# Performance work log

Measured on AMD Instinct MI355X. Metric: run time of the kernel, lower is better.

The kernel has to match this reference:

```python
import jax, jax.numpy as jnp
import numpy as np

B, S, D = 1, 2048, 2048
H, G, HD = 32, 8, 64        # n_heads, n_kv_groups, head_dim
GS = H // G                  # group_size
ROPE_BASE = 10000.0


def _rope_tables(seq_len, head_dim):
    inv_freq = 1.0 / (ROPE_BASE ** (jnp.arange(0, head_dim, 2, dtype=jnp.float32) / head_dim))
    angles = jnp.arange(seq_len, dtype=jnp.float32)[:, None] * inv_freq[None, :]  # [S, HD/2]
    angles = jnp.concatenate([angles, angles], axis=-1)                            # [S, HD]
    return jnp.cos(angles), jnp.sin(angles)


def setup_inputs() -> dict:
    key = jax.random.key(0)
    ks = jax.random.split(key, 5)
    x = jax.random.normal(ks[0], (B, S, D), dtype=jnp.float32)
    mask = jnp.triu(jnp.ones((S, S), dtype=bool), k=1)  # True = masked (causal)
    cos_vals, sin_vals = _rope_tables(S, HD)
    scale = 0.02
    Wq = jax.random.normal(ks[1], (H * HD, D), dtype=jnp.float32) * scale
    Wk = jax.random.normal(ks[2], (G * HD, D), dtype=jnp.float32) * scale
    Wv = jax.random.normal(ks[3], (G * HD, D), dtype=jnp.float32) * scale
    Wo = jax.random.normal(ks[4], (D, H * HD), dtype=jnp.float32) * scale
    return {"x": x, "mask": mask, "cos_vals": cos_vals, "sin_vals": sin_vals,
            "Wq": Wq, "Wk": Wk, "Wv": Wv, "Wo": Wo}


def _apply_rope(t, cos, sin):
    # t: [b, heads, S, HD]; cos/sin: [S, HD]
    half = t.shape[-1] // 2
    t1, t2 = t[..., :half], t[..., half:]
    rotated = jnp.concatenate([-t2, t1], axis=-1)
    return t * cos[None, None] + rotated * sin[None, None]


def reference(x, mask, cos_vals, sin_vals, Wq, Wk, Wv, Wo):
    b, s, _ = x.shape
    q = (x @ Wq.T).reshape(b, s, H, HD).transpose(0, 2, 1, 3)   # [b,H,S,HD]
    k = (x @ Wk.T).reshape(b, s, G, HD).transpose(0, 2, 1, 3)   # [b,G,S,HD]
    v = (x @ Wv.T).reshape(b, s, G, HD).transpose(0, 2, 1, 3)   # [b,G,S,HD]
    q = _apply_rope(q, cos_vals, sin_vals)
    k = _apply_rope(k, cos_vals, sin_vals)
    # Group-broadcast instead of repeat_interleave (same math)
    q = q.reshape(b, G, GS, s, HD)
    scores = jnp.einsum('bghqd,bgkd->bghqk', q, k)              # [b,G,GS,S,S]
    scores = jnp.where(mask[None, None, None], -jnp.inf, scores)
    weights = jax.nn.softmax(scores / np.sqrt(HD).astype(np.float32), axis=-1)
    out = jnp.einsum('bghqk,bgkd->bghqd', weights, v)           # [b,G,GS,S,HD]
    out = out.reshape(b, H, s, HD).transpose(0, 2, 1, 3).reshape(b, s, H * HD)
    return out @ Wo.T
```

## Files before the change

### kernel.cpp

```cpp
#include <hip/hip_runtime.h>
#include <cstddef>
#include <cstdint>

#define S 2048
#define Dm 2048
#define NH 32
#define NG 8
#define HD 64

typedef __attribute__((ext_vector_type(8))) short bf16x8;
typedef __attribute__((ext_vector_type(4))) short bf16x4;
typedef __attribute__((ext_vector_type(4))) float f32x4;

__device__ __forceinline__ float fast_exp2(float x) { return __builtin_amdgcn_exp2f(x); }

__device__ __forceinline__ unsigned short f2bf(float f) {
  unsigned int u = __builtin_bit_cast(unsigned int, f);
  u = (u + 0x7fffu + ((u >> 16) & 1u)) >> 16;
  return (unsigned short)u;
}
__device__ __forceinline__ unsigned int pk2bf(float lo, float hi) {
  unsigned int a = __builtin_bit_cast(unsigned int, lo) + 0x8000u;
  unsigned int b = __builtin_bit_cast(unsigned int, hi) + 0x8000u;
  return (a >> 16) | (b & 0xffff0000u);
}
__device__ __forceinline__ void gl_lds16(const unsigned short* g, unsigned short* l) {
  __builtin_amdgcn_global_load_lds(
      (const __attribute__((address_space(1))) unsigned int*)g,
      (__attribute__((address_space(3))) unsigned int*)l, 16, 0, 0);
}

#define QSC 0.1803368801111601f

__global__ __launch_bounds__(256) void cvt_all(const float* __restrict__ x,
                                               const float* __restrict__ Wq,
                                               const float* __restrict__ Wk,
                                               const float* __restrict__ Wv,
                                               const float* __restrict__ Wo,
                                               unsigned short* __restrict__ xb,
                                               unsigned short* __restrict__ Wcat,
                                               unsigned short* __restrict__ Wob) {
  int i = blockIdx.x * 256 + threadIdx.x;
  const float4* src;
  ushort4* dst;
  if (i < 1048576)      { src = (const float4*)x  + i;             dst = (ushort4*)xb + i; }
  else if (i < 2097152) { src = (const float4*)Wq + (i - 1048576); dst = (ushort4*)Wcat + (i - 1048576); }
  else if (i < 2359296) { src = (const float4*)Wk + (i - 2097152); dst = (ushort4*)Wcat + 1048576 + (i - 2097152); }
  else if (i < 2621440) { src = (const float4*)Wv + (i - 2359296); dst = (ushort4*)Wcat + 1310720 + (i - 2359296); }
  else                  { src = (const float4*)Wo + (i - 2621440); dst = (ushort4*)Wob + (i - 2621440); }
  float4 v = *src;
  ushort4 o;
  o.x = f2bf(v.x); o.y = f2bf(v.y); o.z = f2bf(v.z); o.w = f2bf(v.w);
  *dst = o;
}

__global__ __launch_bounds__(256) void gemm_bf16(const unsigned short* __restrict__ A,
                                                 const unsigned short* __restrict__ B,
                                                 float* __restrict__ Cf,
                                                 unsigned short* __restrict__ Cb,
                                                 unsigned short* __restrict__ VtOut,
                                                 const float* __restrict__ cosv,
                                                 const float* __restrict__ sinv,
                                                 int M, int N, int K) {
  __shared__ __align__(16) unsigned short As[64 * 64];
  __shared__ __align__(16) unsigned short Bs[128 * 64];
  const int tid = threadIdx.x;
  const int lane = tid & 63, wave = tid >> 6;
  const int row0 = blockIdx.y * 64, col0 = blockIdx.x * 128;
  const int wr = (wave >> 1) * 32, wc = (wave & 1) * 64;

  f32x4 acc[2][4];
#pragma unroll
  for (int i = 0; i < 2; i++)
#pragma unroll
    for (int j = 0; j < 4; j++) acc[i][j] = (f32x4){0.f, 0.f, 0.f, 0.f};

  const int arow0 = tid >> 3, aslot0 = ((tid & 7) ^ (arow0 & 7)) * 8;
  const int arow1 = (tid + 256) >> 3, aslot1 = (((tid + 256) & 7) ^ (arow1 & 7)) * 8;
  const int fr = lane & 15, q4 = lane >> 4;

  for (int k0 = 0; k0 < K; k0 += 64) {
    gl_lds16(&A[(size_t)(row0 + arow0) * K + k0 + aslot0], &As[tid * 8]);
    gl_lds16(&A[(size_t)(row0 + arow1) * K + k0 + aslot1], &As[(tid + 256) * 8]);
#pragma unroll
    for (int b = 0; b < 4; b++) {
      int p = tid + b * 256;
      int r = p >> 3, sl = ((p & 7) ^ (r & 7)) * 8;
      gl_lds16(&B[(size_t)(col0 + r) * K + k0 + sl], &Bs[p * 8]);
    }
    __syncthreads();
#pragma unroll
    for (int kk = 0; kk < 2; kk++) {
      bf16x8 af[2], bfr[4];
#pragma unroll
      for (int i = 0; i < 2; i++) {
        int R = wr + i * 16 + fr;
        af[i] = *(const bf16x8*)&As[R * 64 + ((q4 + kk * 4) ^ (R & 7)) * 8];
      }
#pragma unroll
      for (int j = 0; j < 4; j++) {
        int R = wc + j * 16 + fr;
        bfr[j] = *(const bf16x8*)&Bs[R * 64 + ((q4 + kk * 4) ^ (R & 7)) * 8];
      }
#pragma unroll
      for (int i = 0; i < 2; i++)
#pragma unroll
        for (int j = 0; j < 4; j++)
          acc[i][j] = __builtin_amdgcn_mfma_f32_16x16x32_bf16(af[i], bfr[j], acc[i][j], 0, 0, 0);
    }
    __syncthreads();
  }

  const int cc = lane & 15, cr = (lane >> 4) * 4;

  if (cosv) {
#pragma unroll
    for (int i = 0; i < 2; i++) {
      int grb = row0 + wr + i * 16 + cr;
#pragma unroll
      for (int j = 0; j < 2; j++) {
        int gc = col0 + wc + j * 16 + cc;
        if (gc < 2560) {
          int d = j * 16 + cc;
          float qs = (gc < 2048) ? QSC : 1.0f;
#pragma unroll
          for (int r = 0; r < 4; r++) {
            float c = cosv[(grb + r) * 64 + d];
            float s = sinv[(grb + r) * 64 + d];
            float t1 = acc[i][j][r], t2 = acc[i][j + 2][r];
            acc[i][j][r]     = (t1 * c - t2 * s) * qs;
            acc[i][j + 2][r] = (t2 * c + t1 * s) * qs;
          }
        }
      }
    }
  }

#pragma unroll
  for (int i = 0; i < 2; i++)
#pragma unroll
    for (int j = 0; j < 4; j++) {
      int gc = col0 + wc + j * 16 + cc;
#pragma unroll
      for (int r = 0; r < 4; r++) {
        int gr = row0 + wr + i * 16 + cr + r;
        if (cosv) {
          if (gc >= 2560) VtOut[(size_t)(gc - 2560) * 2048 + gr] = f2bf(acc[i][j][r]);
          else            Cb[(size_t)gr * N + gc] = f2bf(acc[i][j][r]);
        } else if (Cf)    Cf[(size_t)gr * N + gc] = acc[i][j][r];
        else              Cb[(size_t)gr * N + gc] = f2bf(acc[i][j][r]);
      }
    }
}

__global__ __launch_bounds__(256, 2) void flash_mfma(const unsigned short* __restrict__ QKV,
                                                     const unsigned short* __restrict__ Vt_g,
                                                     unsigned short* __restrict__ Ob) {
  __shared__ __align__(16) unsigned short Ks[64 * 64];
  __shared__ __align__(16) unsigned short Vs[64 * 64];

  const int tid = threadIdx.x;
  const int lane = tid & 63, wave = tid >> 6;
  const int m15 = lane & 15, q4 = lane >> 4;

  const int L = blockIdx.x;
  const int h = L & 31, g = h >> 2;
  const int u0 = L >> 5, a = u0 >> 3, b = u0 & 7;
  const int u = (a == 0) ? 15 - b : b;
  const int qb = u * 128;
  const int ntiles = 2 * u + 2;

  bf16x8 qf[2][2];
#pragma unroll
  for (int f = 0; f < 2; f++) {
    const size_t qrow = (size_t)(qb + f * 64 + wave * 16 + m15) * 3072 + h * 64;
    qf[f][0] = *(const bf16x8*)&QKV[qrow + q4 * 8];
    qf[f][1] = *(const bf16x8*)&QKV[qrow + 32 + q4 * 8];
  }

  f32x4 accO[2][4];
  float l_i[2] = {0.f, 0.f};
#pragma unroll
  for (int f = 0; f < 2; f++)
#pragma unroll
    for (int v = 0; v < 4; v++) accO[f][v] = (f32x4){0.f, 0.f, 0.f, 0.f};

  const int p0 = wave * 128 + lane, p1 = p0 + 64;
  const int sr0 = p0 >> 3, so0 = ((p0 & 7) ^ (sr0 & 7)) * 8;
  const int sr1 = p1 >> 3, so1 = ((p1 & 7) ^ (sr1 & 7)) * 8;

  for (int t = 0; t < ntiles; t++) {
    const int k0 = t * 64;
    gl_lds16(&QKV[(size_t)(k0 + sr0) * 3072 + 2048 + g * 64 + so0], &Ks[p0 * 8]);
    gl_lds16(&QKV[(size_t)(k0 + sr1) * 3072 + 2048 + g * 64 + so1], &Ks[p1 * 8]);
    gl_lds16(&Vt_g[(size_t)(g * 64 + sr0) * 2048 + k0 + so0], &Vs[p0 * 8]);
    gl_lds16(&Vt_g[(size_t)(g * 64 + sr1) * 2048 + k0 + so1], &Vs[p1 * 8]);
    __syncthreads();

    const bool act0 = (t < ntiles - 1);

    f32x4 sc[2][4];
#pragma unroll
    for (int kt = 0; kt < 4; kt++) {
      const int krow = kt * 16 + m15;
      bf16x8 kf0 = *(const bf16x8*)&Ks[krow * 64 + (q4 ^ (krow & 7)) * 8];
      bf16x8 kf1 = *(const bf16x8*)&Ks[krow * 64 + ((q4 + 4) ^ (krow & 7)) * 8];
      f32x4 z1 = (f32x4){0.f, 0.f, 0.f, 0.f};
      z1 = __builtin_amdgcn_mfma_f32_16x16x32_bf16(kf0, qf[1][0], z1, 0, 0, 0);
      sc[1][kt] = __builtin_amdgcn_mfma_f32_16x16x32_bf16(kf1, qf[1][1], z1, 0, 0, 0);
      if (act0) {
        f32x4 z0 = (f32x4){0.f, 0.f, 0.f, 0.f};
        z0 = __builtin_amdgcn_mfma_f32_16x16x32_bf16(kf0, qf[0][0], z0, 0, 0, 0);
        sc[0][kt] = __builtin_amdgcn_mfma_f32_16x16x32_bf16(kf1, qf[0][1], z0, 0, 0, 0);
      }
    }

    bf16x8 pA0[2], pA1[2];
#pragma unroll
    for (int f = 0; f < 2; f++) {
      if (f == 0 && !act0) continue;
      if (t == 2 * u + f) {
        const int qo = wave * 16 + m15;
#pragma unroll
        for (int kt = 0; kt < 4; kt++)
#pragma unroll
          for (int r = 0; r < 4; r++)
            if (kt * 16 + q4 * 4 + r > qo) sc[f][kt][r] = -1e30f;
      }
      float rs = 0.f;
#pragma unroll
      for (int kt = 0; kt < 4; kt++)
#pragma unroll
        for (int r = 0; r < 4; r++) {
          float p = fast_exp2(sc[f][kt][r]);
          sc[f][kt][r] = p;
          rs += p;
        }
      rs += __shfl_xor(rs, 16);
      rs += __shfl_xor(rs, 32);
      l_i[f] += rs;

      int4 pa0, pa1;
      pa0.x = pk2bf(sc[f][0][0], sc[f][0][1]); pa0.y = pk2bf(sc[f][0][2], sc[f][0][3]);
      pa0.z = pk2bf(sc[f][1][0], sc[f][1][1]); pa0.w = pk2bf(sc[f][1][2], sc[f][1][3]);
      pa1.x = pk2bf(sc[f][2][0], sc[f][2][1]); pa1.y = pk2bf(sc[f][2][2], sc[f][2][3]);
      pa1.z = pk2bf(sc[f][3][0], sc[f][3][1]); pa1.w = pk2bf(sc[f][3][2], sc[f][3][3]);
      pA0[f] = __builtin_bit_cast(bf16x8, pa0);
      pA1[f] = __builtin_bit_cast(bf16x8, pa1);
    }

#pragma unroll
    for (int vt = 0; vt < 4; vt++) {
      const int vrow = vt * 16 + m15;
      const int base = vrow * 64, sw = vrow & 7, half = (q4 & 1) * 4, c1 = q4 >> 1;
      bf16x4 w00 = *(const bf16x4*)&Vs[base + (c1 ^ sw) * 8 + half];
      bf16x4 w01 = *(const bf16x4*)&Vs[base + ((c1 + 2) ^ sw) * 8 + half];
      bf16x4 w10 = *(const bf16x4*)&Vs[base + ((c1 + 4) ^ sw) * 8 + half];
      bf16x4 w11 = *(const bf16x4*)&Vs[base + ((c1 + 6) ^ sw) * 8 + half];
      bf16x8 vB0 = __builtin_shufflevector(w00, w01, 0, 1, 2, 3, 4, 5, 6, 7);
      bf16x8 vB1 = __builtin_shufflevector(w10, w11, 0, 1, 2, 3, 4, 5, 6, 7);
      accO[1][vt] = __builtin_amdgcn_mfma_f32_16x16x32_bf16(pA0[1], vB0, accO[1][vt], 0, 0, 0);
      accO[1][vt] = __builtin_amdgcn_mfma_f32_16x16x32_bf16(pA1[1], vB1, accO[1][vt], 0, 0, 0);
      if (act0) {
        accO[0][vt] = __builtin_amdgcn_mfma_f32_16x16x32_bf16(pA0[0], vB0, accO[0][vt], 0, 0, 0);
        accO[0][vt] = __builtin_amdgcn_mfma_f32_16x16x32_bf16(pA1[0], vB1, accO[0][vt], 0, 0, 0);
      }
    }
    __syncthreads();
  }

#pragma unroll
  for (int f = 0; f < 2; f++) {
    float lr[4];
#pragma unroll
    for (int r = 0; r < 4; r++) lr[r] = 1.0f / __shfl(l_i[f], q4 * 20 + r);
#pragma unroll
    for (int vt = 0; vt < 4; vt++)
#pragma unroll
      for (int r = 0; r < 4; r++) {
        int row = qb + f * 64 + wave * 16 + q4 * 4 + r;
        Ob[(size_t)row * 2048 + h * 64 + vt * 16 + m15] = f2bf(accO[f][vt][r] * lr[r]);
      }
  }
}

extern "C" void kernel_launch(void* const* d_in, const int* in_sizes, int n_in,
                              void* d_out, int out_size, void* d_ws, size_t ws_size,
                              hipStream_t stream) {
  const float* x    = (const float*)d_in[0];
  const float* cosv = (const float*)d_in[2];
  const float* sinv = (const float*)d_in[3];
  const float* Wq   = (const float*)d_in[4];
  const float* Wk   = (const float*)d_in[5];
  const float* Wv   = (const float*)d_in[6];
  const float* Wo   = (const float*)d_in[7];
  float* out = (float*)d_out;

  unsigned short* xb   = (unsigned short*)d_ws;
  unsigned short* Wcat = xb + (size_t)2048 * 2048;
  unsigned short* Wob  = Wcat + (size_t)3072 * 2048;
  unsigned short* QKV  = Wob + (size_t)2048 * 2048;
  unsigned short* Vt_g = QKV + (size_t)3072 * 2048;

  dim3 blk(256);
  cvt_all<<<14336, blk, 0, stream>>>(x, Wq, Wk, Wv, Wo, xb, Wcat, Wob);
  gemm_bf16<<<dim3(24, 32), blk, 0, stream>>>(xb, Wcat, nullptr, QKV, Vt_g, cosv, sinv, 2048, 3072, 2048);
  flash_mfma<<<512, blk, 0, stream>>>(QKV, Vt_g, xb);
  gemm_bf16<<<dim3(16, 32), blk, 0, stream>>>(xb, Wob, out, nullptr, nullptr, nullptr, nullptr, 2048, 2048, 2048);
}
```

Baseline: 230.0 us.

## Double-buffer K/V tiles in flash attention and defer row-sum reduction

Splits the K and V shared-memory tiles into two buffers and prefetches tile t+2 while tile t is being computed. Manual vmcnt waits and raw s_barrier replace __syncthreads, which is meant to hide global-to-LDS load latency behind the MFMA and softmax work. The per-tile cross-lane shuffle reduction of the softmax row sum now happens once at the end instead of every tile. This doubles LDS use per block, which may limit occupancy, and correctness depends on the hand-written vmcnt counts.

```diff
diff --git a/kernel.cpp b/kernel.cpp
--- a/kernel.cpp
+++ b/kernel.cpp
@@ -156,8 +156,8 @@
 __global__ __launch_bounds__(256, 2) void flash_mfma(const unsigned short* __restrict__ QKV,
                                                      const unsigned short* __restrict__ Vt_g,
                                                      unsigned short* __restrict__ Ob) {
-  __shared__ __align__(16) unsigned short Ks[64 * 64];
-  __shared__ __align__(16) unsigned short Vs[64 * 64];
+  __shared__ __align__(16) unsigned short Ks[2][64 * 64];
+  __shared__ __align__(16) unsigned short Vs[2][64 * 64];
 
   const int tid = threadIdx.x;
   const int lane = tid & 63, wave = tid >> 6;
@@ -179,7 +179,7 @@
   }
 
   f32x4 accO[2][4];
-  float l_i[2] = {0.f, 0.f};
+  float l_lane[2] = {0.f, 0.f};
 #pragma unroll
   for (int f = 0; f < 2; f++)
 #pragma unroll
@@ -189,22 +189,30 @@
   const int sr0 = p0 >> 3, so0 = ((p0 & 7) ^ (sr0 & 7)) * 8;
   const int sr1 = p1 >> 3, so1 = ((p1 & 7) ^ (sr1 & 7)) * 8;
 
+#pragma unroll
+  for (int t = 0; t < 2; t++) {
+    const int k0 = t * 64;
+    gl_lds16(&QKV[(size_t)(k0 + sr0) * 3072 + 2048 + g * 64 + so0], &Ks[t][p0 * 8]);
+    gl_lds16(&QKV[(size_t)(k0 + sr1) * 3072 + 2048 + g * 64 + so1], &Ks[t][p1 * 8]);
+    gl_lds16(&Vt_g[(size_t)(g * 64 + sr0) * 2048 + k0 + so0], &Vs[t][p0 * 8]);
+    gl_lds16(&Vt_g[(size_t)(g * 64 + sr1) * 2048 + k0 + so1], &Vs[t][p1 * 8]);
+  }
+
   for (int t = 0; t < ntiles; t++) {
-    const int k0 = t * 64;
-    gl_lds16(&QKV[(size_t)(k0 + sr0) * 3072 + 2048 + g * 64 + so0], &Ks[p0 * 8]);
-    gl_lds16(&QKV[(size_t)(k0 + sr1) * 3072 + 2048 + g * 64 + so1], &Ks[p1 * 8]);
-    gl_lds16(&Vt_g[(size_t)(g * 64 + sr0) * 2048 + k0 + so0], &Vs[p0 * 8]);
-    gl_lds16(&Vt_g[(size_t)(g * 64 + sr1) * 2048 + k0 + so1], &Vs[p1 * 8]);
-    __syncthreads();
-
+    if (t + 1 < ntiles) asm volatile("s_waitcnt vmcnt(4)" ::: "memory");
+    else                asm volatile("s_waitcnt vmcnt(0)" ::: "memory");
+    asm volatile("s_barrier" ::: "memory");
+
+    const unsigned short* Kb = Ks[t & 1];
+    const unsigned short* Vb = Vs[t & 1];
     const bool act0 = (t < ntiles - 1);
 
     f32x4 sc[2][4];
 #pragma unroll
     for (int kt = 0; kt < 4; kt++) {
       const int krow = kt * 16 + m15;
-      bf16x8 kf0 = *(const bf16x8*)&Ks[krow * 64 + (q4 ^ (krow & 7)) * 8];
-      bf16x8 kf1 = *(const bf16x8*)&Ks[krow * 64 + ((q4 + 4) ^ (krow & 7)) * 8];
+      bf16x8 kf0 = *(const bf16x8*)&Kb[krow * 64 + (q4 ^ (krow & 7)) * 8];
+      bf16x8 kf1 = *(const bf16x8*)&Kb[krow * 64 + ((q4 + 4) ^ (krow & 7)) * 8];
       f32x4 z1 = (f32x4){0.f, 0.f, 0.f, 0.f};
       z1 = __builtin_amdgcn_mfma_f32_16x16x32_bf16(kf0, qf[1][0], z1, 0, 0, 0);
       sc[1][kt] = __builtin_amdgcn_mfma_f32_16x16x32_bf16(kf1, qf[1][1], z1, 0, 0, 0);
@@ -236,9 +244,7 @@
           sc[f][kt][r] = p;
           rs += p;
         }
-      rs += __shfl_xor(rs, 16);
-      rs += __shfl_xor(rs, 32);
-      l_i[f] += rs;
+      l_lane[f] += rs;
 
       int4 pa0, pa1;
       pa0.x = pk2bf(sc[f][0][0], sc[f][0][1]); pa0.y = pk2bf(sc[f][0][2], sc[f][0][3]);
@@ -253,10 +259,10 @@
     for (int vt = 0; vt < 4; vt++) {
       const int vrow = vt * 16 + m15;
       const int base = vrow * 64, sw = vrow & 7, half = (q4 & 1) * 4, c1 = q4 >> 1;
-      bf16x4 w00 = *(const bf16x4*)&Vs[base + (c1 ^ sw) * 8 + half];
-      bf16x4 w01 = *(const bf16x4*)&Vs[base + ((c1 + 2) ^ sw) * 8 + half];
-      bf16x4 w10 = *(const bf16x4*)&Vs[base + ((c1 + 4) ^ sw) * 8 + half];
-      bf16x4 w11 = *(const bf16x4*)&Vs[base + ((c1 + 6) ^ sw) * 8 + half];
+      bf16x4 w00 = *(const bf16x4*)&Vb[base + (c1 ^ sw) * 8 + half];
+      bf16x4 w01 = *(const bf16x4*)&Vb[base + ((c1 + 2) ^ sw) * 8 + half];
+      bf16x4 w10 = *(const bf16x4*)&Vb[base + ((c1 + 4) ^ sw) * 8 + half];
+      bf16x4 w11 = *(const bf16x4*)&Vb[base + ((c1 + 6) ^ sw) * 8 + half];
       bf16x8 vB0 = __builtin_shufflevector(w00, w01, 0, 1, 2, 3, 4, 5, 6, 7);
       bf16x8 vB1 = __builtin_shufflevector(w10, w11, 0, 1, 2, 3, 4, 5, 6, 7);
       accO[1][vt] = __builtin_amdgcn_mfma_f32_16x16x32_bf16(pA0[1], vB0, accO[1][vt], 0, 0, 0);
@@ -266,14 +272,27 @@
         accO[0][vt] = __builtin_amdgcn_mfma_f32_16x16x32_bf16(pA1[0], vB1, accO[0][vt], 0, 0, 0);
       }
     }
-    __syncthreads();
+
+    asm volatile("s_barrier" ::: "memory");
+    if (t + 2 < ntiles) {
+      const int k2 = (t + 2) * 64;
+      unsigned short* Kn = (unsigned short*)Ks[t & 1];
+      unsigned short* Vn = (unsigned short*)Vs[t & 1];
+      gl_lds16(&QKV[(size_t)(k2 + sr0) * 3072 + 2048 + g * 64 + so0], &Kn[p0 * 8]);
+      gl_lds16(&QKV[(size_t)(k2 + sr1) * 3072 + 2048 + g * 64 + so1], &Kn[p1 * 8]);
+      gl_lds16(&Vt_g[(size_t)(g * 64 + sr0) * 2048 + k2 + so0], &Vn[p0 * 8]);
+      gl_lds16(&Vt_g[(size_t)(g * 64 + sr1) * 2048 + k2 + so1], &Vn[p1 * 8]);
+    }
   }
 
 #pragma unroll
   for (int f = 0; f < 2; f++) {
+    float lsum = l_lane[f];
+    lsum += __shfl_xor(lsum, 16);
+    lsum += __shfl_xor(lsum, 32);
     float lr[4];
 #pragma unroll
-    for (int r = 0; r < 4; r++) lr[r] = 1.0f / __shfl(l_i[f], q4 * 20 + r);
+    for (int r = 0; r < 4; r++) lr[r] = 1.0f / __shfl(lsum, q4 * 20 + r);
 #pragma unroll
     for (int vt = 0; vt < 4; vt++)
 #pragma unroll
```

Result: faster. 220.1 us (-4.3%).
